# Kernel tuning notes

Measured on AMD Instinct MI355X. Metric: run time of the kernel, lower is better.

Reference implementation:

```python
import jax, jax.numpy as jnp
import numpy as np

EPS_L2 = 1e-6
EPS_RMS = 1e-6

def _dw_causal(x, w):
    # depthwise causal conv: x [B,L,C], w [C,K] (torch Conv1d weight [C,1,K] squeezed)
    K = w.shape[1]
    L = x.shape[1]
    xp = jnp.pad(x, ((0, 0), (K - 1, 0), (0, 0)))
    out = jnp.zeros_like(x)
    for j in range(K):  # K=4, fixed small kernel
        out = out + w[:, j] * xp[:, j:j + L, :]
    return out

def _qkv_conv(x, dw, pw):
    # depthwise causal conv -> pointwise 1x1 conv -> SiLU
    return jax.nn.silu(_dw_causal(x, dw) @ pw.T)

def _l2n(x):
    return x / (jnp.linalg.norm(x, axis=-1, keepdims=True) + EPS_L2)

def setup_inputs() -> dict:
    key = jax.random.key(0)
    B, L, D, M, P, K = 2, 1024, 2048, 2048, 8, 4
    ks = jax.random.split(key, 16)
    inp = {}
    inp['x'] = jax.random.normal(ks[0], (B, L, D), dtype=jnp.float32)
    inp['Wq'] = jax.random.normal(ks[1], (M, D), dtype=jnp.float32) * 0.02
    inp['Wk'] = jax.random.normal(ks[2], (M, D), dtype=jnp.float32) * 0.02
    inp['Wv'] = jax.random.normal(ks[3], (M, D), dtype=jnp.float32) * 0.02
    inp['q_dw'] = jax.random.normal(ks[4], (M, K), dtype=jnp.float32) * 0.1
    inp['k_dw'] = jax.random.normal(ks[5], (M, K), dtype=jnp.float32) * 0.1
    inp['v_dw'] = jax.random.normal(ks[6], (M, K), dtype=jnp.float32) * 0.1
    inp['q_pw'] = jax.random.normal(ks[7], (M, M), dtype=jnp.float32) * 0.02
    inp['k_pw'] = jax.random.normal(ks[8], (M, M), dtype=jnp.float32) * 0.02
    inp['v_pw'] = jax.random.normal(ks[9], (M, M), dtype=jnp.float32) * 0.02
    inp['pk'] = jax.random.normal(ks[10], (P, M), dtype=jnp.float32) * 0.02
    inp['pv'] = jax.random.normal(ks[11], (P, M), dtype=jnp.float32) * 0.02
    inp['mlp_w1'] = jnp.eye(M, dtype=jnp.float32) * 0.1
    inp['mlp_w2'] = jnp.eye(M, dtype=jnp.float32) * 0.1
    inp['eta_w'] = jnp.zeros((1, D), dtype=jnp.float32)
    inp['eta_b'] = jnp.full((1,), 2.0, dtype=jnp.float32)
    inp['theta_w'] = jnp.zeros((1, D), dtype=jnp.float32)
    inp['theta_b'] = jnp.full((1,), -1.0, dtype=jnp.float32)
    inp['alpha_w'] = jnp.zeros((1, D), dtype=jnp.float32)
    inp['alpha_b'] = jnp.full((1,), -2.0, dtype=jnp.float32)
    inp['gate_w'] = jax.random.normal(ks[12], (M, M), dtype=jnp.float32) * 0.02
    inp['gate_b'] = jnp.zeros((M,), dtype=jnp.float32)
    inp['out_w'] = jax.random.normal(ks[13], (D, M), dtype=jnp.float32) * 0.02
    inp['ln_w'] = jnp.ones((D,), dtype=jnp.float32)
    inp['mem_state'] = jnp.zeros((M, M), dtype=jnp.float32)
    inp['sur_state'] = jnp.zeros((M, M), dtype=jnp.float32)
    return inp

def reference(x, Wq, Wk, Wv, q_dw, q_pw, k_dw, k_pw, v_dw, v_pw, pk, pv,
              mlp_w1, mlp_w2, eta_w, eta_b, theta_w, theta_b, alpha_w, alpha_b,
              gate_w, gate_b, out_w, ln_w, mem_state, sur_state):
    B, L, D = x.shape
    M = Wq.shape[0]
    P = pk.shape[0]
    # projections + causal depthwise-separable convs + SiLU
    q = _qkv_conv(x @ Wq.T, q_dw, q_pw)
    k = _qkv_conv(x @ Wk.T, k_dw, k_pw)
    v = _qkv_conv(x @ Wv.T, v_dw, v_pw)
    q = _l2n(q)
    k = _l2n(k)
    # data-dependent eta/theta/alpha from mean-pooled input, scalarized
    x_pooled = x.mean(axis=1)  # [B, D]
    eta = jax.nn.sigmoid(x_pooled @ eta_w.T + eta_b).mean()
    theta = jax.nn.sigmoid(x_pooled @ theta_w.T + theta_b).mean()
    alpha = jax.nn.sigmoid(x_pooled @ alpha_w.T + alpha_b).mean()
    # persistent memory tokens
    pk_n = _l2n(pk)
    k_wp = jnp.concatenate([jnp.broadcast_to(pk_n[None], (B, P, M)), k], axis=1)
    v_wp = jnp.concatenate([jnp.broadcast_to(pv[None], (B, P, M)), v], axis=1)
    # test-time memory update (torch.no_grad block -> stop_gradient)
    pred = jnp.einsum('blm,mh->blh', k, mem_state)
    err = v - pred
    momentary = jnp.einsum('bld,blh->dh', k, err) / (B * L)
    new_surprise = eta * sur_state + theta * momentary
    new_memory = (1.0 - alpha) * mem_state + new_surprise
    snapshot = jax.lax.stop_gradient(new_memory)
    # retrieval: linear memory + deep memory MLP
    linear_ret = jnp.einsum('blm,mh->blh', q, snapshot)
    mlp_ret = jax.nn.silu(q @ mlp_w1.T) @ mlp_w2.T
    retrieved = linear_ret + mlp_ret
    # causal attention with always-visible persistent tokens
    scores = jnp.einsum('blm,bpm->blp', q, k_wp) / jnp.sqrt(jnp.float32(M))
    col = jnp.arange(P + L)
    row = jnp.arange(L)
    mask = (col[None, :] < P) | ((col[None, :] - P) <= row[:, None])  # [L, P+L]
    scores = jnp.where(mask[None], scores, -jnp.inf)
    attn = jax.nn.softmax(scores.astype(jnp.float32), axis=-1).astype(x.dtype)
    context = jnp.einsum('blp,bpm->blm', attn, v_wp)
    retrieved = retrieved + context
    # gated output projection + residual + RMSNorm
    gate = jax.nn.sigmoid(retrieved @ gate_w.T + gate_b)
    out = x + (gate * retrieved) @ out_w.T
    rms = jnp.sqrt(jnp.mean(out * out, axis=-1, keepdims=True) + EPS_RMS)
    return (out / rms) * ln_w
```

## Files before the change

kernel.cpp:

```cpp
#include <hip/hip_runtime.h>
#include <hip/hip_bf16.h>


#define NROWS 2048
#define MD    2048
#define PL    1032
#define PLP   1152
#define NM    4194304

using bf16x8 = __attribute__((ext_vector_type(8))) __bf16;
using f32x4  = __attribute__((ext_vector_type(4))) float;
using u16x8  = __attribute__((ext_vector_type(8))) unsigned short;

__device__ __forceinline__ unsigned short f2bf(float f) {
    union { float f; unsigned int u; } c; c.f = f;
    unsigned int u = c.u;
    return (unsigned short)((u + 0x7fffu + ((u >> 16) & 1u)) >> 16);
}
__device__ __forceinline__ float bf2f(unsigned short h) {
    union { float f; unsigned int u; } c; c.u = ((unsigned int)h) << 16;
    return c.f;
}
__device__ __forceinline__ float ldf(const float* p) { return *p; }
__device__ __forceinline__ float ldf(const unsigned short* p) { return bf2f(*p); }
__device__ __forceinline__ float sigm(float x) { return 1.f / (1.f + __expf(-x)); }
__device__ __forceinline__ float silu(float x) { return x / (1.f + __expf(-x)); }

__device__ __forceinline__ float block_reduce_sum(float v) {
    __shared__ float ws[4];
    #pragma unroll
    for (int o = 32; o > 0; o >>= 1) v += __shfl_down(v, o);
    __syncthreads();
    if ((threadIdx.x & 63) == 0) ws[threadIdx.x >> 6] = v;
    __syncthreads();
    return (ws[0] + ws[1]) + (ws[2] + ws[3]);
}
__device__ __forceinline__ float block_reduce_max(float v) {
    __shared__ float wm[4];
    #pragma unroll
    for (int o = 32; o > 0; o >>= 1) v = fmaxf(v, __shfl_down(v, o));
    __syncthreads();
    if ((threadIdx.x & 63) == 0) wm[threadIdx.x >> 6] = v;
    __syncthreads();
    return fmaxf(fmaxf(wm[0], wm[1]), fmaxf(wm[2], wm[3]));
}

__device__ __forceinline__ void load_lds16(const unsigned short* g, unsigned short* l) {
    __builtin_amdgcn_global_load_lds(
        (const __attribute__((address_space(1))) unsigned int*)g,
        (__attribute__((address_space(3))) unsigned int*)l, 16, 0, 0);
}
__device__ __forceinline__ void raw_barrier() {
    __asm__ volatile("" ::: "memory");
    __builtin_amdgcn_s_barrier();
    __asm__ volatile("" ::: "memory");
}

__global__ __launch_bounds__(256) void gemm_nt(
    const unsigned short* __restrict__ A, const unsigned short* __restrict__ Bm,
    void* __restrict__ Cv, int Mc, int K, long sA, long sB, long sC, int epi)
{
    __shared__ unsigned short As[2][8192];
    __shared__ unsigned short Bs[2][4096];
    const int tid = threadIdx.x, lane = tid & 63, w = tid >> 6;
    const int l16 = lane & 15, quad = lane >> 4;
    const int wr = (w >> 1) * 64, wc = (w & 1) * 32;
    const long rowBase = (long)blockIdx.y * 128;
    const long colBase = (long)blockIdx.x * 64;
    const unsigned short* Ap = A + (long)blockIdx.z * sA;
    const unsigned short* Bp = Bm + (long)blockIdx.z * sB;
    const int r8 = lane >> 3;
    const int cg = (lane & 7) ^ r8;

    const unsigned short* gA[4]; const unsigned short* gB[2];
    unsigned short* lA[4]; unsigned short* lB[2];
    #pragma unroll
    for (int t = 0; t < 4; ++t) {
        int ch = w * 4 + t;
        gA[t] = Ap + (rowBase + ch * 8 + r8) * (long)K + cg * 8;
        lA[t] = &As[0][ch * 512];
    }
    #pragma unroll
    for (int t = 0; t < 2; ++t) {
        int ch = w * 2 + t;
        gB[t] = Bp + (colBase + ch * 8 + r8) * (long)K + cg * 8;
        lB[t] = &Bs[0][ch * 512];
    }

    f32x4 acc[4][2] = {};
    #pragma unroll
    for (int t = 0; t < 4; ++t) { load_lds16(gA[t], lA[t]); gA[t] += 64; }
    #pragma unroll
    for (int t = 0; t < 2; ++t) { load_lds16(gB[t], lB[t]); gB[t] += 64; }

    const int nIter = K >> 6;
    for (int it = 0; it < nIter; ++it) {
        const int cb = it & 1;
        if (it + 1 < nIter) {
            const int nb = cb ^ 1;
            #pragma unroll
            for (int t = 0; t < 4; ++t) { load_lds16(gA[t], lA[t] + nb * 8192); gA[t] += 64; }
            #pragma unroll
            for (int t = 0; t < 2; ++t) { load_lds16(gB[t], lB[t] + nb * 4096); gB[t] += 64; }
            __builtin_amdgcn_s_waitcnt(0xF76);
        } else {
            __builtin_amdgcn_s_waitcnt(0xF70);
        }
        raw_barrier();
        const unsigned short* Ac = As[cb];
        const unsigned short* Bc = Bs[cb];
        #pragma unroll
        for (int ks = 0; ks < 2; ++ks) {
            const int cl = ((ks * 4 + quad) ^ (l16 & 7)) * 8;
            bf16x8 af[4], bfr[2];
            #pragma unroll
            for (int i = 0; i < 4; ++i)
                af[i] = *(const bf16x8*)&Ac[(wr + i * 16 + l16) * 64 + cl];
            #pragma unroll
            for (int j = 0; j < 2; ++j)
                bfr[j] = *(const bf16x8*)&Bc[(wc + j * 16 + l16) * 64 + cl];
            #pragma unroll
            for (int i = 0; i < 4; ++i)
                #pragma unroll
                for (int j = 0; j < 2; ++j)
                    acc[i][j] = __builtin_amdgcn_mfma_f32_16x16x32_bf16(af[i], bfr[j], acc[i][j], 0, 0, 0);
        }
        raw_barrier();
    }

    float* Cf = (float*)Cv + (long)blockIdx.z * sC;
    unsigned short* Ch = (unsigned short*)Cv + (long)blockIdx.z * sC;
    #pragma unroll
    for (int i = 0; i < 4; ++i)
        #pragma unroll
        for (int r = 0; r < 4; ++r) {
            long gr = rowBase + wr + i * 16 + quad * 4 + r;
            #pragma unroll
            for (int j = 0; j < 2; ++j) {
                long gc = colBase + wc + j * 16 + l16;
                long off = gr * (long)Mc + gc;
                float v = acc[i][j][r];
                if (epi == 0)      Cf[off] = v;
                else if (epi == 1) Cf[off] += v;
                else if (epi == 2) Ch[off] = f2bf(v);
                else               Ch[off] = f2bf(silu(v));
            }
        }
}

template <typename TS>
__global__ void k_transpose(const TS* __restrict__ src, unsigned short* __restrict__ dst,
                            int R, int C, int dstLd, int dstOff, long sSrc, long sDst)
{
    __shared__ float tile[32][33];
    const TS* sp = src + (long)blockIdx.z * sSrc;
    unsigned short* dp = dst + (long)blockIdx.z * sDst;
    int c0 = blockIdx.x * 32, r0 = blockIdx.y * 32;
    int tx = threadIdx.x, ty = threadIdx.y;
    #pragma unroll
    for (int i = 0; i < 4; ++i)
        tile[ty + i * 8][tx] = ldf(&sp[(long)(r0 + ty + i * 8) * C + c0 + tx]);
    __syncthreads();
    #pragma unroll
    for (int i = 0; i < 4; ++i)
        dp[(long)(c0 + ty + i * 8) * dstLd + dstOff + r0 + tx] = f2bf(tile[tx][ty + i * 8]);
}

__global__ void k_errT_kT(const unsigned short* __restrict__ vf, const float* __restrict__ pred,
                          const unsigned short* __restrict__ k_bf, unsigned short* __restrict__ eT)
{
    __shared__ float tile[32][33];
    int z = blockIdx.z;
    int c0 = blockIdx.x * 32, r0 = blockIdx.y * 32;
    int tx = threadIdx.x, ty = threadIdx.y;
    #pragma unroll
    for (int i = 0; i < 4; ++i) {
        long idx = (long)(r0 + ty + i * 8) * MD + c0 + tx;
        tile[ty + i * 8][tx] = (z == 0) ? (bf2f(vf[idx]) - pred[idx]) : bf2f(k_bf[idx]);
    }
    __syncthreads();
    unsigned short* dst = eT + (long)z * NM;
    #pragma unroll
    for (int i = 0; i < 4; ++i)
        dst[(long)(c0 + ty + i * 8) * MD + r0 + tx] = f2bf(tile[tx][ty + i * 8]);
}

__global__ void k_snapT(const float* __restrict__ mem, const float* __restrict__ sur,
                        const float* __restrict__ momT, const float* __restrict__ scal,
                        unsigned short* __restrict__ dst)
{
    __shared__ float tile[32][33];
    float eta = scal[0], theta = scal[1], alpha = scal[2];
    int h0 = blockIdx.y * 32, d0 = blockIdx.x * 32;
    int tx = threadIdx.x, ty = threadIdx.y;
    #pragma unroll
    for (int i = 0; i < 4; ++i) {
        long idx = (long)(d0 + ty + i * 8) * MD + h0 + tx;
        tile[ty + i * 8][tx] = (1.f - alpha) * mem[idx] + eta * sur[idx];
    }
    __syncthreads();
    #pragma unroll
    for (int i = 0; i < 4; ++i) {
        long oidx = (long)(h0 + ty + i * 8) * MD + d0 + tx;
        dst[oidx] = f2bf(tile[tx][ty + i * 8] + theta * (1.f / 2048.f) * momT[oidx]);
    }
}

__global__ void k_cvt_multi(const float* s0, const float* s1, const float* s2, const float* s3,
                            const float* s4, const float* s5, const float* s6, const float* s7,
                            unsigned short* d0, unsigned short* d1, unsigned short* d2, unsigned short* d3,
                            unsigned short* d4, unsigned short* d5, unsigned short* d6, unsigned short* d7)
{
    int seg = blockIdx.x >> 11;
    const float* s; unsigned short* d;
    switch (seg) {
        case 0: s = s0; d = d0; break;  case 1: s = s1; d = d1; break;
        case 2: s = s2; d = d2; break;  case 3: s = s3; d = d3; break;
        case 4: s = s4; d = d4; break;  case 5: s = s5; d = d5; break;
        case 6: s = s6; d = d6; break;  default: s = s7; d = d7; break;
    }
    long idx = ((long)(blockIdx.x & 2047) * 256 + threadIdx.x) * 8;
    float4 a = *(const float4*)(s + idx);
    float4 b = *(const float4*)(s + idx + 4);
    u16x8 o;
    o[0] = f2bf(a.x); o[1] = f2bf(a.y); o[2] = f2bf(a.z); o[3] = f2bf(a.w);
    o[4] = f2bf(b.x); o[5] = f2bf(b.y); o[6] = f2bf(b.z); o[7] = f2bf(b.w);
    *(u16x8*)(d + idx) = o;
}

__global__ void k_dwconv(const unsigned short* __restrict__ tproj,
                         const float* __restrict__ qdw, const float* __restrict__ kdw,
                         const float* __restrict__ vdw, unsigned short* __restrict__ conv)
{
    long u = (long)blockIdx.x * 256 + threadIdx.x;
    long flat = u * 8;
    int z = (int)(flat >> 22);
    int rem = (int)(flat & (NM - 1));
    int n = rem >> 11, m = rem & 2047;
    int l = n & 1023;
    const float* dw = (z == 0) ? qdw : (z == 1) ? kdw : vdw;
    const unsigned short* src = tproj + (long)n * 6144 + z * 2048 + m;
    float4 dwv[8];
    #pragma unroll
    for (int e = 0; e < 8; ++e) dwv[e] = *(const float4*)(dw + (m + e) * 4);
    float acc[8] = {};
    #pragma unroll
    for (int j = 0; j < 4; ++j) {
        int dl = j - 3;
        if (l + dl >= 0) {
            u16x8 r = *(const u16x8*)(src + (long)dl * 6144);
            #pragma unroll
            for (int e = 0; e < 8; ++e)
                acc[e] += ((const float*)&dwv[e])[j] * bf2f(r[e]);
        }
    }
    u16x8 o;
    #pragma unroll
    for (int e = 0; e < 8; ++e) o[e] = f2bf(acc[e]);
    *(u16x8*)(conv + (long)z * NM + (long)n * 2048 + m) = o;
}

__global__ void k_post_qkv(const float* __restrict__ t_big, unsigned short* __restrict__ q_bf,
                           unsigned short* __restrict__ k_bf, unsigned short* __restrict__ vf,
                           unsigned short* __restrict__ kwp)
{
    int bid = blockIdx.x, z = bid >> 11, n = bid & 2047;
    const float* row = t_big + (long)z * NM + (long)n * 2048;
    int t = threadIdx.x;
    float4 a = *(const float4*)(row + t * 8);
    float4 b = *(const float4*)(row + t * 8 + 4);
    float v[8] = {silu(a.x), silu(a.y), silu(a.z), silu(a.w),
                  silu(b.x), silu(b.y), silu(b.z), silu(b.w)};
    if (z == 2) {
        u16x8 o;
        #pragma unroll
        for (int e = 0; e < 8; ++e) o[e] = f2bf(v[e]);
        *(u16x8*)(vf + (long)n * 2048 + t * 8) = o;
        return;
    }
    float ss = 0.f;
    #pragma unroll
    for (int e = 0; e < 8; ++e) ss += v[e] * v[e];
    ss = block_reduce_sum(ss);
    float inv = 1.f / (sqrtf(ss) + 1e-6f);
    u16x8 o;
    #pragma unroll
    for (int e = 0; e < 8; ++e) o[e] = f2bf(v[e] * inv);
    if (z == 0) {
        *(u16x8*)(q_bf + (long)n * 2048 + t * 8) = o;
    } else {
        *(u16x8*)(k_bf + (long)n * 2048 + t * 8) = o;
        int bb = n >> 10, l = n & 1023;
        *(u16x8*)(kwp + ((long)bb * PLP + 8 + l) * MD + t * 8) = o;
    }
}

__global__ void k_misc(const float* __restrict__ pk, const float* __restrict__ pv,
                       unsigned short* __restrict__ kwp, unsigned short* __restrict__ vwpT)
{
    int bid = blockIdx.x, t = threadIdx.x;
    if (bid < 8) {
        const float* row = pk + bid * MD;
        float4 a = *(const float4*)(row + t * 8);
        float4 b = *(const float4*)(row + t * 8 + 4);
        float v[8] = {a.x, a.y, a.z, a.w, b.x, b.y, b.z, b.w};
        float ss = 0.f;
        #pragma unroll
        for (int e = 0; e < 8; ++e) ss += v[e] * v[e];
        ss = block_reduce_sum(ss);
        float inv = 1.f / (sqrtf(ss) + 1e-6f);
        u16x8 o;
        #pragma unroll
        for (int e = 0; e < 8; ++e) o[e] = f2bf(v[e] * inv);
        *(u16x8*)(kwp + (long)bid * MD + t * 8) = o;
        *(u16x8*)(kwp + (long)PLP * MD + (long)bid * MD + t * 8) = o;
    } else if (bid < 72) {
        int i = (bid - 8) * 256 + t;
        int m = i >> 3, pp = i & 7;
        unsigned short h = f2bf(pv[pp * MD + m]);
        vwpT[(long)m * PLP + pp] = h;
        vwpT[(long)MD * PLP + (long)m * PLP + pp] = h;
    } else if (bid < 312) {
        long flat = ((long)(bid - 72) * 256 + t) * 8;
        int b = (int)(flat / 245760);
        int r = (int)(flat % 245760);
        int j = 1032 + (r >> 11), m = r & 2047;
        u16x8 zz = {};
        *(u16x8*)(kwp + ((long)b * PLP + j) * MD + m) = zz;
    } else {
        long flat = ((long)(bid - 312) * 256 + t) * 8;
        int bm = (int)(flat / 120);
        int o = (int)(flat % 120);
        u16x8 zz = {};
        *(u16x8*)(vwpT + (long)bm * PLP + 1032 + o) = zz;
    }
}

__global__ void k_pooled(const float* __restrict__ x, const float* __restrict__ ew,
                         const float* __restrict__ tw, const float* __restrict__ aw,
                         float* __restrict__ dots) {
    int b = blockIdx.y;
    long base = (long)b * 1024 * MD;
    long start = (long)blockIdx.x * 8192;
    float s0 = 0, s1 = 0, s2 = 0;
    for (int s = 0; s < 32; ++s) {
        long f = start + threadIdx.x + (long)s * 256;
        float xv = x[base + f];
        int d = (int)(f & (MD - 1));
        s0 += xv * ew[d]; s1 += xv * tw[d]; s2 += xv * aw[d];
    }
    s0 = block_reduce_sum(s0);
    if (threadIdx.x == 0) atomicAdd(&dots[0 + b], s0);
    s1 = block_reduce_sum(s1);
    if (threadIdx.x == 0) atomicAdd(&dots[2 + b], s1);
    s2 = block_reduce_sum(s2);
    if (threadIdx.x == 0) atomicAdd(&dots[4 + b], s2);
}
__global__ void k_scal_fin(const float* __restrict__ dots, const float* __restrict__ eb,
                           const float* __restrict__ tb, const float* __restrict__ ab,
                           float* __restrict__ scal) {
    if (threadIdx.x == 0 && blockIdx.x == 0) {
        const float invL = 1.f / 1024.f;
        float e = 0, th = 0, al = 0;
        for (int b = 0; b < 2; ++b) {
            e  += sigm(dots[0 + b] * invL + eb[0]);
            th += sigm(dots[2 + b] * invL + tb[0]);
            al += sigm(dots[4 + b] * invL + ab[0]);
        }
        scal[0] = e * 0.5f; scal[1] = th * 0.5f; scal[2] = al * 0.5f;
    }
}

__global__ void k_silu8(const float* __restrict__ in, unsigned short* __restrict__ o) {
    long i = ((long)blockIdx.x * 256 + threadIdx.x) * 8;
    float4 a = *(const float4*)(in + i);
    float4 b = *(const float4*)(in + i + 4);
    u16x8 r;
    r[0] = f2bf(silu(a.x)); r[1] = f2bf(silu(a.y)); r[2] = f2bf(silu(a.z)); r[3] = f2bf(silu(a.w));
    r[4] = f2bf(silu(b.x)); r[5] = f2bf(silu(b.y)); r[6] = f2bf(silu(b.z)); r[7] = f2bf(silu(b.w));
    *(u16x8*)(o + i) = r;
}
__global__ void k_addcvt(const float* __restrict__ a, const float* __restrict__ b,
                         unsigned short* __restrict__ o) {
    long i = ((long)blockIdx.x * 256 + threadIdx.x) * 8;
    float4 a0 = *(const float4*)(a + i), a1 = *(const float4*)(a + i + 4);
    float4 b0 = *(const float4*)(b + i), b1 = *(const float4*)(b + i + 4);
    u16x8 r;
    r[0] = f2bf(a0.x + b0.x); r[1] = f2bf(a0.y + b0.y); r[2] = f2bf(a0.z + b0.z); r[3] = f2bf(a0.w + b0.w);
    r[4] = f2bf(a1.x + b1.x); r[5] = f2bf(a1.y + b1.y); r[6] = f2bf(a1.z + b1.z); r[7] = f2bf(a1.w + b1.w);
    *(u16x8*)(o + i) = r;
}
__global__ void k_gate8(const float* __restrict__ pre, const float* __restrict__ gb,
                        const float* __restrict__ ret, const float* __restrict__ mlp2,
                        unsigned short* __restrict__ o) {
    long i = ((long)blockIdx.x * 256 + threadIdx.x) * 8;
    int m = (int)(i & (MD - 1));
    float4 p0 = *(const float4*)(pre + i),  p1 = *(const float4*)(pre + i + 4);
    float4 r0 = *(const float4*)(ret + i),  r1 = *(const float4*)(ret + i + 4);
    float4 q0 = *(const float4*)(mlp2 + i), q1 = *(const float4*)(mlp2 + i + 4);
    float4 g0 = *(const float4*)(gb + m),   g1 = *(const float4*)(gb + m + 4);
    u16x8 r;
    r[0] = f2bf(sigm(p0.x + g0.x) * (r0.x + q0.x));
    r[1] = f2bf(sigm(p0.y + g0.y) * (r0.y + q0.y));
    r[2] = f2bf(sigm(p0.z + g0.z) * (r0.z + q0.z));
    r[3] = f2bf(sigm(p0.w + g0.w) * (r0.w + q0.w));
    r[4] = f2bf(sigm(p1.x + g1.x) * (r1.x + q1.x));
    r[5] = f2bf(sigm(p1.y + g1.y) * (r1.y + q1.y));
    r[6] = f2bf(sigm(p1.z + g1.z) * (r1.z + q1.z));
    r[7] = f2bf(sigm(p1.w + g1.w) * (r1.w + q1.w));
    *(u16x8*)(o + i) = r;
}

__global__ void k_softmax(const float* __restrict__ S, unsigned short* __restrict__ attn) {
    int l = blockIdx.x, b = blockIdx.y;
    long base = ((long)b * 1024 + l) * PLP;
    int nvis = 8 + l + 1;
    const float scale = 0.022097086912079608f;
    int t = threadIdx.x;
    float vals[5];
    float mx = -1e30f;
    #pragma unroll
    for (int s = 0; s < 5; ++s) {
        int j = t + s * 256;
        float v = -1e30f;
        if (j < nvis) v = S[base + j] * scale;
        vals[s] = v;
        mx = fmaxf(mx, v);
    }
    mx = block_reduce_max(mx);
    float sum = 0.f;
    #pragma unroll
    for (int s = 0; s < 5; ++s) {
        int j = t + s * 256;
        float e = 0.f;
        if (j < nvis) e = __expf(vals[s] - mx);
        vals[s] = e; sum += e;
    }
    sum = block_reduce_sum(sum);
    float inv = 1.f / sum;
    #pragma unroll
    for (int s = 0; s < 5; ++s) {
        int j = t + s * 256;
        if (j < PLP) attn[base + j] = f2bf(vals[s] * inv);
    }
}

__global__ void k_final(const float* __restrict__ x, const float* __restrict__ y,
                        const float* __restrict__ lnw, float* __restrict__ out) {
    int n = blockIdx.x;
    long base = (long)n * MD;
    int t = threadIdx.x;
    float4 a0 = *(const float4*)(x + base + t * 8), a1 = *(const float4*)(x + base + t * 8 + 4);
    float4 b0 = *(const float4*)(y + base + t * 8), b1 = *(const float4*)(y + base + t * 8 + 4);
    float v[8] = {a0.x + b0.x, a0.y + b0.y, a0.z + b0.z, a0.w + b0.w,
                  a1.x + b1.x, a1.y + b1.y, a1.z + b1.z, a1.w + b1.w};
    float ss = 0.f;
    #pragma unroll
    for (int e = 0; e < 8; ++e) ss += v[e] * v[e];
    ss = block_reduce_sum(ss);
    float inv = rsqrtf(ss * (1.f / 2048.f) + 1e-6f);
    float4 w0 = *(const float4*)(lnw + t * 8), w1 = *(const float4*)(lnw + t * 8 + 4);
    float4 o0 = {v[0] * inv * w0.x, v[1] * inv * w0.y, v[2] * inv * w0.z, v[3] * inv * w0.w};
    float4 o1 = {v[4] * inv * w1.x, v[5] * inv * w1.y, v[6] * inv * w1.z, v[7] * inv * w1.w};
    *(float4*)(out + base + t * 8) = o0;
    *(float4*)(out + base + t * 8 + 4) = o1;
}

static inline void gemm(hipStream_t st, const void* A, const void* B, void* C,
                        int Mc, int K, long sA, long sB, long sC,
                        int gx, int gy, int gz, int epi) {
    hipLaunchKernelGGL(gemm_nt, dim3(gx, gy, gz), dim3(256), 0, st,
                       (const unsigned short*)A, (const unsigned short*)B, C,
                       Mc, K, sA, sB, sC, epi);
}

extern "C" void kernel_launch(void* const* d_in, const int* in_sizes, int n_in,
                              void* d_out, int out_size, void* d_ws, size_t ws_size,
                              hipStream_t stream) {
    const float* x    = (const float*)d_in[0];
    const float* Wq   = (const float*)d_in[1];
    const float* Wk   = (const float*)d_in[2];
    const float* Wv   = (const float*)d_in[3];
    const float* qdw  = (const float*)d_in[4];
    const float* kdw  = (const float*)d_in[5];
    const float* vdw  = (const float*)d_in[6];
    const float* qpw  = (const float*)d_in[7];
    const float* kpw  = (const float*)d_in[8];
    const float* vpw  = (const float*)d_in[9];
    const float* pk   = (const float*)d_in[10];
    const float* pv   = (const float*)d_in[11];
    const float* mw1  = (const float*)d_in[12];
    const float* mw2  = (const float*)d_in[13];
    const float* etaw = (const float*)d_in[14];
    const float* etab = (const float*)d_in[15];
    const float* thw  = (const float*)d_in[16];
    const float* thb  = (const float*)d_in[17];
    const float* alw  = (const float*)d_in[18];
    const float* alb  = (const float*)d_in[19];
    const float* gw   = (const float*)d_in[20];
    const float* gb   = (const float*)d_in[21];
    const float* ow   = (const float*)d_in[22];
    const float* lnw  = (const float*)d_in[23];
    const float* mem  = (const float*)d_in[24];
    const float* sur  = (const float*)d_in[25];
    float* out = (float*)d_out;

    char* ws = (char*)d_ws;
    const size_t MB = 1024 * 1024;
    float* dots = (float*)ws;
    float* scal = (float*)(ws + 1024);
    float*          t0f  = (float*)(ws + 4096);
    float*          t1f  = t0f + NM;
    float*          t2f  = t0f + 2 * NM;
    unsigned short* tproj = (unsigned short*)t0f;
    float*          retf = (float*)(ws + 4096 + 48 * MB);
    unsigned short* k_bf = (unsigned short*)(ws + 4096 + 64 * MB);
    unsigned short* q_bf = k_bf + NM;
    unsigned short* qc   = k_bf + 2 * NM;
    unsigned short* g_bf = k_bf;
    unsigned short* x_bf = (unsigned short*)(ws + 4096 + 88 * MB);
    unsigned short* vf   = x_bf;
    unsigned short* attn = x_bf;
    unsigned short* wQKV = (unsigned short*)(ws + 4096 + 96 * MB);
    unsigned short* conv = wQKV;
    unsigned short* kwp  = wQKV;
    unsigned short* vwpT = kwp + (long)2 * PLP * MD;
    unsigned short* wPW  = (unsigned short*)(ws + 4096 + 120 * MB);
    unsigned short* eT   = wPW;
    unsigned short* kT   = eT + NM;
    unsigned short* gw_bf = wPW;
    unsigned short* ow_bf = wPW + NM;
    unsigned short* wMem  = (unsigned short*)(ws + 4096 + 144 * MB);
    unsigned short* wMlp1 = wMem + NM;
    unsigned short* wSnap = wMem;
    unsigned short* wMlp2 = wMem + NM;

    const dim3 b256(256);
    const dim3 bT(32, 8);

    hipMemsetAsync(dots, 0, 256, stream);
    hipLaunchKernelGGL(k_pooled, dim3(256, 2), b256, 0, stream, x, etaw, thw, alw, dots);
    hipLaunchKernelGGL(k_scal_fin, dim3(1), dim3(64), 0, stream, dots, etab, thb, alb, scal);
    hipLaunchKernelGGL(k_cvt_multi, dim3(16384), b256, 0, stream,
                       x, Wq, Wk, Wv, qpw, kpw, vpw, mw1,
                       x_bf, wQKV, wQKV + NM, wQKV + 2 * (long)NM,
                       wPW, wPW + NM, wPW + 2 * (long)NM, wMlp1);
    hipLaunchKernelGGL(k_transpose<float>, dim3(64, 64, 1), bT, 0, stream,
                       mem, wMem, MD, MD, MD, 0, 0L, 0L);
    gemm(stream, x_bf, wQKV, tproj, 6144, MD, 0, 0, 0, 96, 16, 1, 2);
    hipLaunchKernelGGL(k_dwconv, dim3(6144), b256, 0, stream, tproj, qdw, kdw, vdw, conv);
    gemm(stream, conv, wPW, t0f, MD, MD, NM, NM, NM, 32, 16, 3, 0);
    hipLaunchKernelGGL(k_misc, dim3(552), b256, 0, stream, pk, pv, kwp, vwpT);
    hipLaunchKernelGGL(k_post_qkv, dim3(6144), b256, 0, stream, t0f, q_bf, k_bf, vf, kwp);
    hipLaunchKernelGGL(k_transpose<unsigned short>, dim3(64, 32, 2), bT, 0, stream,
                       vf, vwpT, 1024, MD, PLP, 8, (long)1024 * MD, (long)MD * PLP);
    gemm(stream, k_bf, wMem, t0f, MD, MD, NM, NM, NM, 32, 16, 2, 0);
    hipLaunchKernelGGL(k_errT_kT, dim3(64, 64, 2), bT, 0, stream, vf, t0f, k_bf, eT);
    hipLaunchKernelGGL(k_silu8, dim3(2048), b256, 0, stream, t1f, qc);
    gemm(stream, eT, kT, t2f, MD, MD, 0, 0, 0, 32, 16, 1, 0);
    hipLaunchKernelGGL(k_snapT, dim3(64, 64), bT, 0, stream, mem, sur, t2f, scal, wSnap);
    hipLaunchKernelGGL(k_cvt_multi, dim3(6144), b256, 0, stream,
                       mw2, gw, ow, mw2, mw2, mw2, mw2, mw2,
                       wMlp2, gw_bf, ow_bf, wMlp2, wMlp2, wMlp2, wMlp2, wMlp2);
    gemm(stream, q_bf, wSnap, retf, MD, MD, NM, NM, (long)(t1f - retf), 32, 16, 2, 0);
    gemm(stream, q_bf, kwp, t2f, PLP, MD,
         (long)1024 * MD, (long)PLP * MD, (long)1024 * PLP, 18, 8, 2, 0);
    hipLaunchKernelGGL(k_softmax, dim3(1024, 2), b256, 0, stream, t2f, attn);
    gemm(stream, attn, vwpT, retf, MD, PLP,
         (long)1024 * PLP, (long)MD * PLP, (long)1024 * MD, 32, 8, 2, 1);
    hipLaunchKernelGGL(k_addcvt, dim3(2048), b256, 0, stream, retf, t1f, qc);
    gemm(stream, qc, gw_bf, t0f, MD, MD, 0, 0, 0, 32, 16, 1, 0);
    hipLaunchKernelGGL(k_gate8, dim3(2048), b256, 0, stream, t0f, gb, retf, t1f, g_bf);
    gemm(stream, g_bf, ow_bf, t0f, MD, MD, 0, 0, 0, 32, 16, 1, 0);
    hipLaunchKernelGGL(k_final, dim3(2048), b256, 0, stream, x, t0f, lnw, out);
}
```

Baseline: 801.8 us.

## Add 128x128 GEMM tile kernel and fuse SiLU into batched GEMM epilogue

Adds a second GEMM kernel with 128x128 output tiles (4x4 MFMA accumulators per wave) and uses it for the large QKV projection, pointwise conv, memory and snapshot GEMMs. The goal is more operand reuse per LDS load and fewer blocks. A per-batch-slice epilogue selector packed into an int, with byte strides, lets one batched launch write fp32 output for one slice and SiLU-bf16 output for another. This removes the separate k_silu8 pass. The larger tiles raise register and LDS use, which may lower occupancy, and cut the grid to fewer blocks relative to the CU count.

Result: faster. 785.9 us (-2.0%).

```diff
diff --git a/kernel.cpp b/kernel.cpp
--- a/kernel.cpp
+++ b/kernel.cpp
@@ -55,10 +55,17 @@
     __builtin_amdgcn_s_barrier();
     __asm__ volatile("" ::: "memory");
 }
+__device__ __forceinline__ void epi_store(int epi, float* Cf, unsigned short* Ch,
+                                          long off, float v) {
+    if (epi == 0)      Cf[off] = v;
+    else if (epi == 1) Cf[off] += v;
+    else if (epi == 2) Ch[off] = f2bf(v);
+    else               Ch[off] = f2bf(silu(v));
+}
 
 __global__ __launch_bounds__(256) void gemm_nt(
     const unsigned short* __restrict__ A, const unsigned short* __restrict__ Bm,
-    void* __restrict__ Cv, int Mc, int K, long sA, long sB, long sC, int epi)
+    void* __restrict__ Cv, int Mc, int K, long sA, long sB, long sCb, int epiPack)
 {
     __shared__ unsigned short As[2][8192];
     __shared__ unsigned short Bs[2][4096];
@@ -69,6 +76,7 @@
     const long colBase = (long)blockIdx.x * 64;
     const unsigned short* Ap = A + (long)blockIdx.z * sA;
     const unsigned short* Bp = Bm + (long)blockIdx.z * sB;
+    const int epi = (epiPack >> (blockIdx.z * 4)) & 15;
     const int r8 = lane >> 3;
     const int cg = (lane & 7) ^ r8;
 
@@ -128,8 +136,9 @@
         raw_barrier();
     }
 
-    float* Cf = (float*)Cv + (long)blockIdx.z * sC;
-    unsigned short* Ch = (unsigned short*)Cv + (long)blockIdx.z * sC;
+    char* Cb = (char*)Cv + (long)blockIdx.z * sCb;
+    float* Cf = (float*)Cb;
+    unsigned short* Ch = (unsigned short*)Cb;
     #pragma unroll
     for (int i = 0; i < 4; ++i)
         #pragma unroll
@@ -138,12 +147,92 @@
             #pragma unroll
             for (int j = 0; j < 2; ++j) {
                 long gc = colBase + wc + j * 16 + l16;
-                long off = gr * (long)Mc + gc;
-                float v = acc[i][j][r];
-                if (epi == 0)      Cf[off] = v;
-                else if (epi == 1) Cf[off] += v;
-                else if (epi == 2) Ch[off] = f2bf(v);
-                else               Ch[off] = f2bf(silu(v));
+                epi_store(epi, Cf, Ch, gr * (long)Mc + gc, acc[i][j][r]);
+            }
+        }
+}
+
+__global__ __launch_bounds__(256) void gemm_nt_big(
+    const unsigned short* __restrict__ A, const unsigned short* __restrict__ Bm,
+    void* __restrict__ Cv, int Mc, int K, long sA, long sB, long sCb, int epiPack)
+{
+    __shared__ unsigned short As[2][8192];
+    __shared__ unsigned short Bs[2][8192];
+    const int tid = threadIdx.x, lane = tid & 63, w = tid >> 6;
+    const int l16 = lane & 15, quad = lane >> 4;
+    const int wr = (w >> 1) * 64, wc = (w & 1) * 64;
+    const long rowBase = (long)blockIdx.y * 128;
+    const long colBase = (long)blockIdx.x * 128;
+    const unsigned short* Ap = A + (long)blockIdx.z * sA;
+    const unsigned short* Bp = Bm + (long)blockIdx.z * sB;
+    const int epi = (epiPack >> (blockIdx.z * 4)) & 15;
+    const int r8 = lane >> 3;
+    const int cg = (lane & 7) ^ r8;
+
+    const unsigned short* gA[4]; const unsigned short* gB[4];
+    unsigned short* lA[4]; unsigned short* lB[4];
+    #pragma unroll
+    for (int t = 0; t < 4; ++t) {
+        int ch = w * 4 + t;
+        gA[t] = Ap + (rowBase + ch * 8 + r8) * (long)K + cg * 8;
+        lA[t] = &As[0][ch * 512];
+        gB[t] = Bp + (colBase + ch * 8 + r8) * (long)K + cg * 8;
+        lB[t] = &Bs[0][ch * 512];
+    }
+
+    f32x4 acc[4][4] = {};
+    #pragma unroll
+    for (int t = 0; t < 4; ++t) { load_lds16(gA[t], lA[t]); gA[t] += 64; }
+    #pragma unroll
+    for (int t = 0; t < 4; ++t) { load_lds16(gB[t], lB[t]); gB[t] += 64; }
+
+    const int nIter = K >> 6;
+    for (int it = 0; it < nIter; ++it) {
+        const int cb = it & 1;
+        if (it + 1 < nIter) {
+            const int nb = cb ^ 1;
+            #pragma unroll
+            for (int t = 0; t < 4; ++t) { load_lds16(gA[t], lA[t] + nb * 8192); gA[t] += 64; }
+            #pragma unroll
+            for (int t = 0; t < 4; ++t) { load_lds16(gB[t], lB[t] + nb * 8192); gB[t] += 64; }
+            __builtin_amdgcn_s_waitcnt(0xF78);
+        } else {
+            __builtin_amdgcn_s_waitcnt(0xF70);
+        }
+        raw_barrier();
+        const unsigned short* Ac = As[cb];
+        const unsigned short* Bc = Bs[cb];
+        #pragma unroll
+        for (int ks = 0; ks < 2; ++ks) {
+            const int cl = ((ks * 4 + quad) ^ (l16 & 7)) * 8;
+            bf16x8 af[4], bfr[4];
+            #pragma unroll
+            for (int i = 0; i < 4; ++i)
+                af[i] = *(const bf16x8*)&Ac[(wr + i * 16 + l16) * 64 + cl];
+            #pragma unroll
+            for (int j = 0; j < 4; ++j)
+                bfr[j] = *(const bf16x8*)&Bc[(wc + j * 16 + l16) * 64 + cl];
+            #pragma unroll
+            for (int i = 0; i < 4; ++i)
+                #pragma unroll
+                for (int j = 0; j < 4; ++j)
+                    acc[i][j] = __builtin_amdgcn_mfma_f32_16x16x32_bf16(af[i], bfr[j], acc[i][j], 0, 0, 0);
+        }
+        raw_barrier();
+    }
+
+    char* Cb = (char*)Cv + (long)blockIdx.z * sCb;
+    float* Cf = (float*)Cb;
+    unsigned short* Ch = (unsigned short*)Cb;
+    #pragma unroll
+    for (int i = 0; i < 4; ++i)
+        #pragma unroll
+        for (int r = 0; r < 4; ++r) {
+            long gr = rowBase + wr + i * 16 + quad * 4 + r;
+            #pragma unroll
+            for (int j = 0; j < 4; ++j) {
+                long gc = colBase + wc + j * 16 + l16;
+                epi_store(epi, Cf, Ch, gr * (long)Mc + gc, acc[i][j][r]);
             }
         }
 }
@@ -371,15 +460,6 @@
     }
 }
 
-__global__ void k_silu8(const float* __restrict__ in, unsigned short* __restrict__ o) {
-    long i = ((long)blockIdx.x * 256 + threadIdx.x) * 8;
-    float4 a = *(const float4*)(in + i);
-    float4 b = *(const float4*)(in + i + 4);
-    u16x8 r;
-    r[0] = f2bf(silu(a.x)); r[1] = f2bf(silu(a.y)); r[2] = f2bf(silu(a.z)); r[3] = f2bf(silu(a.w));
-    r[4] = f2bf(silu(b.x)); r[5] = f2bf(silu(b.y)); r[6] = f2bf(silu(b.z)); r[7] = f2bf(silu(b.w));
-    *(u16x8*)(o + i) = r;
-}
 __global__ void k_addcvt(const float* __restrict__ a, const float* __restrict__ b,
                          unsigned short* __restrict__ o) {
     long i = ((long)blockIdx.x * 256 + threadIdx.x) * 8;
@@ -466,12 +546,19 @@
     *(float4*)(out + base + t * 8 + 4) = o1;
 }
 
-static inline void gemm(hipStream_t st, const void* A, const void* B, void* C,
-                        int Mc, int K, long sA, long sB, long sC,
-                        int gx, int gy, int gz, int epi) {
+static inline void gemm64(hipStream_t st, const void* A, const void* B, void* C,
+                          int Mc, int K, long sA, long sB, long sCb,
+                          int gx, int gy, int gz, int epiPack) {
     hipLaunchKernelGGL(gemm_nt, dim3(gx, gy, gz), dim3(256), 0, st,
                        (const unsigned short*)A, (const unsigned short*)B, C,
-                       Mc, K, sA, sB, sC, epi);
+                       Mc, K, sA, sB, sCb, epiPack);
+}
+static inline void gemm128(hipStream_t st, const void* A, const void* B, void* C,
+                           int Mc, int K, long sA, long sB, long sCb,
+                           int gx, int gy, int gz, int epiPack) {
+    hipLaunchKernelGGL(gemm_nt_big, dim3(gx, gy, gz), dim3(256), 0, st,
+                       (const unsigned short*)A, (const unsigned short*)B, C,
+                       Mc, K, sA, sB, sCb, epiPack);
 }
 
 extern "C" void kernel_launch(void* const* d_in, const int* in_sizes, int n_in,
@@ -547,30 +634,31 @@
                        wPW, wPW + NM, wPW + 2 * (long)NM, wMlp1);
     hipLaunchKernelGGL(k_transpose<float>, dim3(64, 64, 1), bT, 0, stream,
                        mem, wMem, MD, MD, MD, 0, 0L, 0L);
-    gemm(stream, x_bf, wQKV, tproj, 6144, MD, 0, 0, 0, 96, 16, 1, 2);
+    gemm128(stream, x_bf, wQKV, tproj, 6144, MD, 0, 0, 0, 48, 16, 1, 2);
     hipLaunchKernelGGL(k_dwconv, dim3(6144), b256, 0, stream, tproj, qdw, kdw, vdw, conv);
-    gemm(stream, conv, wPW, t0f, MD, MD, NM, NM, NM, 32, 16, 3, 0);
+    gemm128(stream, conv, wPW, t0f, MD, MD, NM, NM, (long)NM * 4, 16, 16, 3, 0);
     hipLaunchKernelGGL(k_misc, dim3(552), b256, 0, stream, pk, pv, kwp, vwpT);
     hipLaunchKernelGGL(k_post_qkv, dim3(6144), b256, 0, stream, t0f, q_bf, k_bf, vf, kwp);
     hipLaunchKernelGGL(k_transpose<unsigned short>, dim3(64, 32, 2), bT, 0, stream,
                        vf, vwpT, 1024, MD, PLP, 8, (long)1024 * MD, (long)MD * PLP);
-    gemm(stream, k_bf, wMem, t0f, MD, MD, NM, NM, NM, 32, 16, 2, 0);
+    gemm128(stream, k_bf, wMem, t0f, MD, MD, NM, NM,
+            (long)((char*)qc - (char*)t0f), 16, 16, 2, 0x30);
     hipLaunchKernelGGL(k_errT_kT, dim3(64, 64, 2), bT, 0, stream, vf, t0f, k_bf, eT);
-    hipLaunchKernelGGL(k_silu8, dim3(2048), b256, 0, stream, t1f, qc);
-    gemm(stream, eT, kT, t2f, MD, MD, 0, 0, 0, 32, 16, 1, 0);
+    gemm64(stream, eT, kT, t2f, MD, MD, 0, 0, 0, 32, 16, 1, 0);
     hipLaunchKernelGGL(k_snapT, dim3(64, 64), bT, 0, stream, mem, sur, t2f, scal, wSnap);
     hipLaunchKernelGGL(k_cvt_multi, dim3(6144), b256, 0, stream,
                        mw2, gw, ow, mw2, mw2, mw2, mw2, mw2,
                        wMlp2, gw_bf, ow_bf, wMlp2, wMlp2, wMlp2, wMlp2, wMlp2);
-    gemm(stream, q_bf, wSnap, retf, MD, MD, NM, NM, (long)(t1f - retf), 32, 16, 2, 0);
-    gemm(stream, q_bf, kwp, t2f, PLP, MD,
-         (long)1024 * MD, (long)PLP * MD, (long)1024 * PLP, 18, 8, 2, 0);
+    gemm128(stream, q_bf, wSnap, retf, MD, MD, NM, NM,
+            (long)((char*)t1f - (char*)retf), 16, 16, 2, 0);
+    gemm64(stream, q_bf, kwp, t2f, PLP, MD,
+           (long)1024 * MD, (long)PLP * MD, (long)1024 * PLP * 4, 18, 8, 2, 0);
     hipLaunchKernelGGL(k_softmax, dim3(1024, 2), b256, 0, stream, t2f, attn);
-    gemm(stream, attn, vwpT, retf, MD, PLP,
-         (long)1024 * PLP, (long)MD * PLP, (long)1024 * MD, 32, 8, 2, 1);
+    gemm64(stream, attn, vwpT, retf, MD, PLP,
+           (long)1024 * PLP, (long)MD * PLP, (long)1024 * MD * 4, 32, 8, 2, 0x11);
     hipLaunchKernelGGL(k_addcvt, dim3(2048), b256, 0, stream, retf, t1f, qc);
-    gemm(stream, qc, gw_bf, t0f, MD, MD, 0, 0, 0, 32, 16, 1, 0);
+    gemm64(stream, qc, gw_bf, t0f, MD, MD, 0, 0, 0, 32, 16, 1, 0);
     hipLaunchKernelGGL(k_gate8, dim3(2048), b256, 0, stream, t0f, gb, retf, t1f, g_bf);
-    gemm(stream, g_bf, ow_bf, t0f, MD, MD, 0, 0, 0, 32, 16, 1, 0);
+    gemm64(stream, g_bf, ow_bf, t0f, MD, MD, 0, 0, 0, 32, 16, 1, 0);
     hipLaunchKernelGGL(k_final, dim3(2048), b256, 0, stream, x, t0f, lnw, out);
 }
```
